# Kernel optimization log

Measured on AMD Instinct MI355X. Metric: run time of the kernel, lower is better.

The kernel has to match this reference:

```python
import jax, jax.numpy as jnp
import numpy as np


def setup_inputs() -> dict:
    key = jax.random.key(0)
    k1, k2 = jax.random.split(key)
    N, C, T, K = 8192, 3, 2048, 10
    Xt = jax.random.normal(k1, (N, C, T), dtype=jnp.float32)
    y_true = jax.random.randint(k2, (N,), 0, K, dtype=jnp.int64)
    return {"Xt": Xt, "y_true": y_true, "num_classes": K}


def reference(Xt, y_true, num_classes):
    # Within-Class Sum of Squares: for each class k,
    #   loss_k = mean((Xk - mean(Xk, axis=0))**2)  (mean over all elements)
    # total = mean over classes. Assumes all num_classes labels are present
    # (matches torch.unique iteration under this data distribution).
    N = Xt.shape[0]
    D = Xt.shape[1] * Xt.shape[2]  # elements per sample
    sums = jax.ops.segment_sum(Xt, y_true, num_segments=num_classes)        # [K, C, T]
    counts = jax.ops.segment_sum(jnp.ones((N,), Xt.dtype), y_true,
                                 num_segments=num_classes)                  # [K]
    means = sums / counts[:, None, None]                                    # [K, C, T]
    sq = jnp.square(Xt - means[y_true])                                     # [N, C, T]
    sq_per_sample = sq.reshape(N, -1).sum(axis=1)                           # [N]
    sq_sums = jax.ops.segment_sum(sq_per_sample, y_true,
                                  num_segments=num_classes)                 # [K]
    per_class_mse = sq_sums / (counts * D)                                  # [K]
    return per_class_mse.mean()
```

## Files before the change

### kernel.cpp

```cpp
#include <hip/hip_runtime.h>

#define N_SAMP 8192
#define D_DIM 6144
#define K_CLS 10
#define CHUNK 32
#define NWIN (N_SAMP / CHUNK)
#define COLS_PER_BLOCK 1024
#define NGROUPS (D_DIM / COLS_PER_BLOCK)
#define PIPE 8

__global__ __launch_bounds__(1024) void build_sort(const int* __restrict__ y,
                                                   int* __restrict__ counts,
                                                   int* __restrict__ sorted) {
    __shared__ int M[K_CLS * 1024];
    __shared__ int wsum[16];
    const int tid = threadIdx.x;
    const int lane = tid & 63;
    const int wid = tid >> 6;

    const int base = tid * 8;
    const int4 ya = ((const int4*)y)[tid * 2];
    const int4 yb = ((const int4*)y)[tid * 2 + 1];
    int yy[8] = {ya.x, ya.y, ya.z, ya.w, yb.x, yb.y, yb.z, yb.w};
    int h[K_CLS];
#pragma unroll
    for (int k = 0; k < K_CLS; ++k) h[k] = 0;
#pragma unroll
    for (int i = 0; i < 8; ++i)
#pragma unroll
        for (int k = 0; k < K_CLS; ++k) h[k] += (yy[i] == k) ? 1 : 0;
#pragma unroll
    for (int k = 0; k < K_CLS; ++k) M[k * 1024 + tid] = h[k];
    __syncthreads();

    int loc[K_CLS];
    int run = 0;
#pragma unroll
    for (int j = 0; j < K_CLS; ++j) { loc[j] = run; run += M[tid * K_CLS + j]; }
    int v = run;
#pragma unroll
    for (int d = 1; d < 64; d <<= 1) {
        int n = __shfl_up(v, d, 64);
        if (lane >= d) v += n;
    }
    if (lane == 63) wsum[wid] = v;
    __syncthreads();
    int wbase = 0;
#pragma unroll
    for (int w = 0; w < 16; ++w) wbase += (w < wid) ? wsum[w] : 0;
    const int tbase = wbase + (v - run);
    __syncthreads();
#pragma unroll
    for (int j = 0; j < K_CLS; ++j) M[tid * K_CLS + j] = tbase + loc[j];
    __syncthreads();

    if (tid < K_CLS) {
        const int s = M[tid * 1024];
        const int e = (tid == K_CLS - 1) ? N_SAMP : M[(tid + 1) * 1024];
        counts[tid] = e - s;
    }

    int off[K_CLS];
#pragma unroll
    for (int k = 0; k < K_CLS; ++k) off[k] = M[k * 1024 + tid];
#pragma unroll
    for (int i = 0; i < 8; ++i)
#pragma unroll
        for (int k = 0; k < K_CLS; ++k)
            if (yy[i] == k) sorted[off[k]++] = (k << 16) | (base + i);
}

__global__ __launch_bounds__(256) void wcss_accum(const float* __restrict__ X,
                                                  const int* __restrict__ sorted,
                                                  float* __restrict__ S1,
                                                  float* __restrict__ s2sum) {
    __shared__ int off_lds[CHUNK];
    __shared__ int cls_lds[CHUNK];
    __shared__ float wred[4];
    const int tid = threadIdx.x;
    const int lane = tid & 63;
    const int wid = tid >> 6;
    const int col0 = blockIdx.x * COLS_PER_BLOCK + tid * 4;

    if (tid < CHUNK) {
        const int p = sorted[blockIdx.y * CHUNK + tid];
        off_lds[tid] = (p & 0xffff) * (D_DIM * (int)sizeof(float));
        cls_lds[tid] = p >> 16;
    }
    __syncthreads();

    const char* basep = (const char*)(X + col0);
    float4 a1 = make_float4(0.f, 0.f, 0.f, 0.f);
    float s2c = 0.f;
    int kcur = __builtin_amdgcn_readfirstlane(cls_lds[0]);

    float4 buf[PIPE];
#pragma unroll
    for (int j = 0; j < PIPE; ++j)
        buf[j] = *(const float4*)(basep + (size_t)off_lds[j]);

#pragma unroll
    for (int s = 0; s < CHUNK; ++s) {
        const float4 v = buf[s & (PIPE - 1)];
        if (s + PIPE < CHUNK)
            buf[s & (PIPE - 1)] =
                *(const float4*)(basep + (size_t)off_lds[s + PIPE]);

        const int yk = __builtin_amdgcn_readfirstlane(cls_lds[s]);
        if (yk != kcur) {
            float* b1 = S1 + kcur * D_DIM + col0;
            atomicAdd(b1 + 0, a1.x); atomicAdd(b1 + 1, a1.y);
            atomicAdd(b1 + 2, a1.z); atomicAdd(b1 + 3, a1.w);
            float r = s2c;
#pragma unroll
            for (int o = 32; o > 0; o >>= 1) r += __shfl_down(r, o, 64);
            if (lane == 0) wred[wid] = r;
            __syncthreads();
            if (tid == 0)
                atomicAdd(&s2sum[kcur], wred[0] + wred[1] + wred[2] + wred[3]);
            __syncthreads();
            a1 = make_float4(0.f, 0.f, 0.f, 0.f);
            s2c = 0.f;
            kcur = yk;
        }
        a1.x += v.x; a1.y += v.y; a1.z += v.z; a1.w += v.w;
        s2c += v.x * v.x + v.y * v.y + v.z * v.z + v.w * v.w;
    }

    float* b1 = S1 + kcur * D_DIM + col0;
    atomicAdd(b1 + 0, a1.x); atomicAdd(b1 + 1, a1.y);
    atomicAdd(b1 + 2, a1.z); atomicAdd(b1 + 3, a1.w);
#pragma unroll
    for (int o = 32; o > 0; o >>= 1) s2c += __shfl_down(s2c, o, 64);
    if (lane == 0) wred[wid] = s2c;
    __syncthreads();
    if (tid == 0)
        atomicAdd(&s2sum[kcur], wred[0] + wred[1] + wred[2] + wred[3]);
}

__global__ __launch_bounds__(256) void wcss_finish(const float* __restrict__ S1,
                                                   const float* __restrict__ s2sum,
                                                   const int* __restrict__ counts,
                                                   float* __restrict__ out) {
    __shared__ float sbuf[256];
    const int tid = threadIdx.x;
    const int k = blockIdx.x / NGROUPS;
    const int g = blockIdx.x % NGROUPS;
    const float cnt = (float)counts[k];
    const float inv = 1.0f / (cnt * cnt * (float)D_DIM * (float)K_CLS);

    const float4 v = *(const float4*)(S1 + k * D_DIM + g * COLS_PER_BLOCK + tid * 4);
    float t = -(v.x * v.x + v.y * v.y + v.z * v.z + v.w * v.w) * inv;
    if (g == 0 && tid == 0)
        t += s2sum[k] / (cnt * (float)D_DIM * (float)K_CLS);

    sbuf[tid] = t;
    __syncthreads();
    for (int off = 128; off > 0; off >>= 1) {
        if (tid < off) sbuf[tid] += sbuf[tid + off];
        __syncthreads();
    }
    if (tid == 0) atomicAdd(out, sbuf[0]);
}

extern "C" void kernel_launch(void* const* d_in, const int* in_sizes, int n_in,
                              void* d_out, int out_size, void* d_ws, size_t ws_size,
                              hipStream_t stream) {
    const float* X = (const float*)d_in[0];
    const int* y = (const int*)d_in[1];

    float* S1 = (float*)d_ws;
    float* s2sum = S1 + K_CLS * D_DIM;
    int* counts = (int*)(s2sum + K_CLS);
    int* sorted = counts + K_CLS;
    float* out = (float*)d_out;

    hipMemsetAsync(S1, 0, (K_CLS * D_DIM + K_CLS) * sizeof(float), stream);
    hipMemsetAsync(out, 0, sizeof(float), stream);

    build_sort<<<dim3(1), dim3(1024), 0, stream>>>(y, counts, sorted);
    wcss_accum<<<dim3(NGROUPS, NWIN), dim3(256), 0, stream>>>(X, sorted, S1, s2sum);
    wcss_finish<<<dim3(K_CLS * NGROUPS), dim3(256), 0, stream>>>(S1, s2sum,
                                                                 counts, out);
}
```

Baseline: 298.3 us.

## Fold memsets into sort kernel and finish via last-block reduction

The two hipMemsetAsync calls are removed and the S1/s2sum zeroing moves into build_sort. The separate finish kernel is dropped in favour of a last-block-done pattern in wcss_accum: an atomic counter picks the final block, which reads S1 with atomic loads and writes the result directly. Loads of X become nontemporal. This cuts launch and memset overhead but serialises the final reduction onto one block of 256 threads reading 61K floats.

```diff
diff --git a/kernel.cpp b/kernel.cpp
--- a/kernel.cpp
+++ b/kernel.cpp
@@ -7,17 +7,33 @@
 #define NWIN (N_SAMP / CHUNK)
 #define COLS_PER_BLOCK 1024
 #define NGROUPS (D_DIM / COLS_PER_BLOCK)
+#define NBLK (NGROUPS * NWIN)
 #define PIPE 8
+
+typedef float f4 __attribute__((ext_vector_type(4)));
 
 __global__ __launch_bounds__(1024) void build_sort(const int* __restrict__ y,
                                                    int* __restrict__ counts,
-                                                   int* __restrict__ sorted) {
+                                                   int* __restrict__ sorted,
+                                                   float* __restrict__ S1,
+                                                   float* __restrict__ s2sum,
+                                                   unsigned* __restrict__ ctr) {
     __shared__ int M[K_CLS * 1024];
     __shared__ int wsum[16];
     const int tid = threadIdx.x;
     const int lane = tid & 63;
     const int wid = tid >> 6;
 
+    {
+        f4 z = {0.f, 0.f, 0.f, 0.f};
+        f4* p = (f4*)S1;
+#pragma unroll
+        for (int i = 0; i < (K_CLS * D_DIM) / (4 * 1024); ++i)
+            p[i * 1024 + tid] = z;
+        if (tid < K_CLS) s2sum[tid] = 0.f;
+        if (tid == K_CLS) *ctr = 0u;
+    }
+
     const int base = tid * 8;
     const int4 ya = ((const int4*)y)[tid * 2];
     const int4 yb = ((const int4*)y)[tid * 2 + 1];
@@ -72,11 +88,15 @@
 
 __global__ __launch_bounds__(256) void wcss_accum(const float* __restrict__ X,
                                                   const int* __restrict__ sorted,
+                                                  const int* __restrict__ counts,
                                                   float* __restrict__ S1,
-                                                  float* __restrict__ s2sum) {
+                                                  float* __restrict__ s2sum,
+                                                  unsigned* __restrict__ ctr,
+                                                  float* __restrict__ out) {
     __shared__ int off_lds[CHUNK];
     __shared__ int cls_lds[CHUNK];
     __shared__ float wred[4];
+    __shared__ int last_s;
     const int tid = threadIdx.x;
     const int lane = tid & 63;
     const int wid = tid >> 6;
@@ -90,21 +110,22 @@
     __syncthreads();
 
     const char* basep = (const char*)(X + col0);
-    float4 a1 = make_float4(0.f, 0.f, 0.f, 0.f);
+    f4 a1 = {0.f, 0.f, 0.f, 0.f};
     float s2c = 0.f;
     int kcur = __builtin_amdgcn_readfirstlane(cls_lds[0]);
 
-    float4 buf[PIPE];
+    f4 buf[PIPE];
 #pragma unroll
     for (int j = 0; j < PIPE; ++j)
-        buf[j] = *(const float4*)(basep + (size_t)off_lds[j]);
+        buf[j] = __builtin_nontemporal_load(
+            (const f4*)(basep + (size_t)off_lds[j]));
 
 #pragma unroll
     for (int s = 0; s < CHUNK; ++s) {
-        const float4 v = buf[s & (PIPE - 1)];
+        const f4 v = buf[s & (PIPE - 1)];
         if (s + PIPE < CHUNK)
-            buf[s & (PIPE - 1)] =
-                *(const float4*)(basep + (size_t)off_lds[s + PIPE]);
+            buf[s & (PIPE - 1)] = __builtin_nontemporal_load(
+                (const f4*)(basep + (size_t)off_lds[s + PIPE]));
 
         const int yk = __builtin_amdgcn_readfirstlane(cls_lds[s]);
         if (yk != kcur) {
@@ -119,11 +140,11 @@
             if (tid == 0)
                 atomicAdd(&s2sum[kcur], wred[0] + wred[1] + wred[2] + wred[3]);
             __syncthreads();
-            a1 = make_float4(0.f, 0.f, 0.f, 0.f);
+            a1 = (f4){0.f, 0.f, 0.f, 0.f};
             s2c = 0.f;
             kcur = yk;
         }
-        a1.x += v.x; a1.y += v.y; a1.z += v.z; a1.w += v.w;
+        a1 += v;
         s2c += v.x * v.x + v.y * v.y + v.z * v.z + v.w * v.w;
     }
 
@@ -136,31 +157,38 @@
     __syncthreads();
     if (tid == 0)
         atomicAdd(&s2sum[kcur], wred[0] + wred[1] + wred[2] + wred[3]);
-}
-
-__global__ __launch_bounds__(256) void wcss_finish(const float* __restrict__ S1,
-                                                   const float* __restrict__ s2sum,
-                                                   const int* __restrict__ counts,
-                                                   float* __restrict__ out) {
-    __shared__ float sbuf[256];
-    const int tid = threadIdx.x;
-    const int k = blockIdx.x / NGROUPS;
-    const int g = blockIdx.x % NGROUPS;
-    const float cnt = (float)counts[k];
-    const float inv = 1.0f / (cnt * cnt * (float)D_DIM * (float)K_CLS);
-
-    const float4 v = *(const float4*)(S1 + k * D_DIM + g * COLS_PER_BLOCK + tid * 4);
-    float t = -(v.x * v.x + v.y * v.y + v.z * v.z + v.w * v.w) * inv;
-    if (g == 0 && tid == 0)
-        t += s2sum[k] / (cnt * (float)D_DIM * (float)K_CLS);
-
-    sbuf[tid] = t;
-    __syncthreads();
-    for (int off = 128; off > 0; off >>= 1) {
-        if (tid < off) sbuf[tid] += sbuf[tid + off];
-        __syncthreads();
-    }
-    if (tid == 0) atomicAdd(out, sbuf[0]);
+
+    __threadfence();
+    if (tid == 0) {
+        unsigned t = atomicAdd(ctr, 1u);
+        last_s = (t == (unsigned)(NBLK - 1)) ? 1 : 0;
+    }
+    __syncthreads();
+    if (!last_s) return;
+    __threadfence();
+
+    float part = 0.f;
+#pragma unroll
+    for (int k = 0; k < K_CLS; ++k) {
+        const float c = (float)counts[k];
+        const float inv2 = 1.0f / (c * c * (float)D_DIM * (float)K_CLS);
+        const float* Sk = S1 + k * D_DIM;
+        for (int j = 0; j < D_DIM / 256; ++j) {
+            float vv = __hip_atomic_load(&Sk[j * 256 + tid], __ATOMIC_RELAXED,
+                                         __HIP_MEMORY_SCOPE_AGENT);
+            part -= vv * vv * inv2;
+        }
+        if (tid == 0)
+            part += __hip_atomic_load(&s2sum[k], __ATOMIC_RELAXED,
+                                      __HIP_MEMORY_SCOPE_AGENT) /
+                    (c * (float)D_DIM * (float)K_CLS);
+    }
+    float r = part;
+#pragma unroll
+    for (int o = 32; o > 0; o >>= 1) r += __shfl_down(r, o, 64);
+    if (lane == 0) wred[wid] = r;
+    __syncthreads();
+    if (tid == 0) *out = wred[0] + wred[1] + wred[2] + wred[3];
 }
 
 extern "C" void kernel_launch(void* const* d_in, const int* in_sizes, int n_in,
@@ -173,13 +201,11 @@
     float* s2sum = S1 + K_CLS * D_DIM;
     int* counts = (int*)(s2sum + K_CLS);
     int* sorted = counts + K_CLS;
+    unsigned* ctr = (unsigned*)(sorted + N_SAMP);
     float* out = (float*)d_out;
 
-    hipMemsetAsync(S1, 0, (K_CLS * D_DIM + K_CLS) * sizeof(float), stream);
-    hipMemsetAsync(out, 0, sizeof(float), stream);
-
-    build_sort<<<dim3(1), dim3(1024), 0, stream>>>(y, counts, sorted);
-    wcss_accum<<<dim3(NGROUPS, NWIN), dim3(256), 0, stream>>>(X, sorted, S1, s2sum);
-    wcss_finish<<<dim3(K_CLS * NGROUPS), dim3(256), 0, stream>>>(S1, s2sum,
-                                                                 counts, out);
+    build_sort<<<dim3(1), dim3(1024), 0, stream>>>(y, counts, sorted,
+                                                   S1, s2sum, ctr);
+    wcss_accum<<<dim3(NGROUPS, NWIN), dim3(256), 0, stream>>>(X, sorted, counts,
+                                                              S1, s2sum, ctr, out);
 }
```

Result: slower. 615.7 us (+106.4%).

## Replace sort-based gather with streaming masked per-class accumulation into partials

Applied to the files above, without the earlier changes.

Drops the counting sort and the gathered row reads. Rows are now streamed contiguously, and each thread keeps per-class accumulators selected by a 0/1 mask. Per-chunk partial sums are written to a workspace buffer and reduced in the finish kernel, which replaces the atomics on S1. The memsets are folded into the histogram kernel. The cost is ten accumulators per thread, which raises register pressure, plus about 31 MB of partial writes and reads.

```diff
diff --git a/kernel.cpp b/kernel.cpp
--- a/kernel.cpp
+++ b/kernel.cpp
@@ -3,25 +3,42 @@
 #define N_SAMP 8192
 #define D_DIM 6144
 #define K_CLS 10
-#define CHUNK 32
-#define NWIN (N_SAMP / CHUNK)
-#define COLS_PER_BLOCK 1024
-#define NGROUPS (D_DIM / COLS_PER_BLOCK)
-#define PIPE 8
+#define RCH 128
+#define ROWS_PER_CH (N_SAMP / RCH)
+#define CGS 2
+#define COLS_PER_CG (D_DIM / CGS)
+#define TPB_S (COLS_PER_CG / 4)
+#define FIN_CG 24
+#define FIN_COLS (D_DIM / FIN_CG)
 
-__global__ __launch_bounds__(1024) void build_sort(const int* __restrict__ y,
+typedef float f4 __attribute__((ext_vector_type(4)));
+
+__device__ __forceinline__ void atom_add_dev(float* p, float v) {
+    __hip_atomic_fetch_add(p, v, __ATOMIC_RELAXED, __HIP_MEMORY_SCOPE_AGENT);
+}
+__device__ __forceinline__ float wave_sum(float x) {
+#pragma unroll
+    for (int o = 32; o > 0; o >>= 1) x += __shfl_down(x, o, 64);
+    return x;
+}
+__device__ __forceinline__ int wave_sum_i(int x) {
+#pragma unroll
+    for (int o = 32; o > 0; o >>= 1) x += __shfl_down(x, o, 64);
+    return x;
+}
+
+__global__ __launch_bounds__(1024) void histo_init(const int* __restrict__ y,
                                                    int* __restrict__ counts,
-                                                   int* __restrict__ sorted) {
-    __shared__ int M[K_CLS * 1024];
-    __shared__ int wsum[16];
+                                                   float* __restrict__ s2sum,
+                                                   float* __restrict__ out) {
+    __shared__ int hred[16][K_CLS];
     const int tid = threadIdx.x;
     const int lane = tid & 63;
     const int wid = tid >> 6;
 
-    const int base = tid * 8;
     const int4 ya = ((const int4*)y)[tid * 2];
     const int4 yb = ((const int4*)y)[tid * 2 + 1];
-    int yy[8] = {ya.x, ya.y, ya.z, ya.w, yb.x, yb.y, yb.z, yb.w};
+    const int yy[8] = {ya.x, ya.y, ya.z, ya.w, yb.x, yb.y, yb.z, yb.w};
     int h[K_CLS];
 #pragma unroll
     for (int k = 0; k < K_CLS; ++k) h[k] = 0;
@@ -30,137 +47,85 @@
 #pragma unroll
         for (int k = 0; k < K_CLS; ++k) h[k] += (yy[i] == k) ? 1 : 0;
 #pragma unroll
-    for (int k = 0; k < K_CLS; ++k) M[k * 1024 + tid] = h[k];
+    for (int k = 0; k < K_CLS; ++k) {
+        const int s = wave_sum_i(h[k]);
+        if (lane == 0) hred[wid][k] = s;
+    }
     __syncthreads();
+    if (tid < K_CLS) {
+        int s = 0;
+#pragma unroll
+        for (int w = 0; w < 16; ++w) s += hred[w][tid];
+        counts[tid] = s;
+        s2sum[tid] = 0.f;
+    }
+    if (tid == K_CLS) *out = 0.f;
+}
 
-    int loc[K_CLS];
-    int run = 0;
+__global__ __launch_bounds__(TPB_S, 3) void wcss_stream(
+        const float* __restrict__ X, const int* __restrict__ y,
+        float* __restrict__ part, float* __restrict__ s2sum) {
+    const int tid = threadIdx.x;
+    const int lane = tid & 63;
+    const int cg = blockIdx.x;
+    const int rc = blockIdx.y;
+    const int col0 = cg * COLS_PER_CG + tid * 4;
+    const int rbase = rc * ROWS_PER_CH;
+
+    f4 acc[K_CLS];
+    float s2[K_CLS];
 #pragma unroll
-    for (int j = 0; j < K_CLS; ++j) { loc[j] = run; run += M[tid * K_CLS + j]; }
-    int v = run;
+    for (int k = 0; k < K_CLS; ++k) { acc[k] = (f4){0.f,0.f,0.f,0.f}; s2[k] = 0.f; }
+
+    const float* xp = X + (size_t)rbase * D_DIM + col0;
+    const int* yp = y + rbase;
+
+#pragma unroll 8
+    for (int r = 0; r < ROWS_PER_CH; ++r) {
+        const int yk = __builtin_amdgcn_readfirstlane(yp[r]);
+        const f4 v = *(const f4*)(xp + (size_t)r * D_DIM);
+        const float dot = v.x*v.x + v.y*v.y + v.z*v.z + v.w*v.w;
 #pragma unroll
-    for (int d = 1; d < 64; d <<= 1) {
-        int n = __shfl_up(v, d, 64);
-        if (lane >= d) v += n;
-    }
-    if (lane == 63) wsum[wid] = v;
-    __syncthreads();
-    int wbase = 0;
-#pragma unroll
-    for (int w = 0; w < 16; ++w) wbase += (w < wid) ? wsum[w] : 0;
-    const int tbase = wbase + (v - run);
-    __syncthreads();
-#pragma unroll
-    for (int j = 0; j < K_CLS; ++j) M[tid * K_CLS + j] = tbase + loc[j];
-    __syncthreads();
-
-    if (tid < K_CLS) {
-        const int s = M[tid * 1024];
-        const int e = (tid == K_CLS - 1) ? N_SAMP : M[(tid + 1) * 1024];
-        counts[tid] = e - s;
+        for (int k = 0; k < K_CLS; ++k) {
+            const float m = (yk == k) ? 1.0f : 0.0f;
+            acc[k] += v * m;
+            s2[k] = fmaf(m, dot, s2[k]);
+        }
     }
 
-    int off[K_CLS];
 #pragma unroll
-    for (int k = 0; k < K_CLS; ++k) off[k] = M[k * 1024 + tid];
+    for (int k = 0; k < K_CLS; ++k)
+        *(f4*)(part + ((size_t)(rc * K_CLS + k)) * D_DIM + col0) = acc[k];
+
 #pragma unroll
-    for (int i = 0; i < 8; ++i)
-#pragma unroll
-        for (int k = 0; k < K_CLS; ++k)
-            if (yy[i] == k) sorted[off[k]++] = (k << 16) | (base + i);
+    for (int k = 0; k < K_CLS; ++k) {
+        const float rs = wave_sum(s2[k]);
+        if (lane == 0) atom_add_dev(&s2sum[k], rs);
+    }
 }
 
-__global__ __launch_bounds__(256) void wcss_accum(const float* __restrict__ X,
-                                                  const int* __restrict__ sorted,
-                                                  float* __restrict__ S1,
-                                                  float* __restrict__ s2sum) {
-    __shared__ int off_lds[CHUNK];
-    __shared__ int cls_lds[CHUNK];
-    __shared__ float wred[4];
+__global__ __launch_bounds__(64) void wcss_finish(const float* __restrict__ part,
+                                                  const float* __restrict__ s2sum,
+                                                  const int* __restrict__ counts,
+                                                  float* __restrict__ out) {
     const int tid = threadIdx.x;
-    const int lane = tid & 63;
-    const int wid = tid >> 6;
-    const int col0 = blockIdx.x * COLS_PER_BLOCK + tid * 4;
+    const int k = blockIdx.x / FIN_CG;
+    const int g = blockIdx.x % FIN_CG;
+    const int col0 = g * FIN_COLS + tid * 4;
+    const float cnt = (float)counts[k];
+    const float invDK = 1.0f / ((float)D_DIM * (float)K_CLS);
 
-    if (tid < CHUNK) {
-        const int p = sorted[blockIdx.y * CHUNK + tid];
-        off_lds[tid] = (p & 0xffff) * (D_DIM * (int)sizeof(float));
-        cls_lds[tid] = p >> 16;
+    f4 S0 = {0.f,0.f,0.f,0.f}, S1v = {0.f,0.f,0.f,0.f};
+#pragma unroll 4
+    for (int rc = 0; rc < RCH; rc += 2) {
+        S0 += *(const f4*)(part + ((size_t)((rc    ) * K_CLS + k)) * D_DIM + col0);
+        S1v += *(const f4*)(part + ((size_t)((rc + 1) * K_CLS + k)) * D_DIM + col0);
     }
-    __syncthreads();
-
-    const char* basep = (const char*)(X + col0);
-    float4 a1 = make_float4(0.f, 0.f, 0.f, 0.f);
-    float s2c = 0.f;
-    int kcur = __builtin_amdgcn_readfirstlane(cls_lds[0]);
-
-    float4 buf[PIPE];
-#pragma unroll
-    for (int j = 0; j < PIPE; ++j)
-        buf[j] = *(const float4*)(basep + (size_t)off_lds[j]);
-
-#pragma unroll
-    for (int s = 0; s < CHUNK; ++s) {
-        const float4 v = buf[s & (PIPE - 1)];
-        if (s + PIPE < CHUNK)
-            buf[s & (PIPE - 1)] =
-                *(const float4*)(basep + (size_t)off_lds[s + PIPE]);
-
-        const int yk = __builtin_amdgcn_readfirstlane(cls_lds[s]);
-        if (yk != kcur) {
-            float* b1 = S1 + kcur * D_DIM + col0;
-            atomicAdd(b1 + 0, a1.x); atomicAdd(b1 + 1, a1.y);
-            atomicAdd(b1 + 2, a1.z); atomicAdd(b1 + 3, a1.w);
-            float r = s2c;
-#pragma unroll
-            for (int o = 32; o > 0; o >>= 1) r += __shfl_down(r, o, 64);
-            if (lane == 0) wred[wid] = r;
-            __syncthreads();
-            if (tid == 0)
-                atomicAdd(&s2sum[kcur], wred[0] + wred[1] + wred[2] + wred[3]);
-            __syncthreads();
-            a1 = make_float4(0.f, 0.f, 0.f, 0.f);
-            s2c = 0.f;
-            kcur = yk;
-        }
-        a1.x += v.x; a1.y += v.y; a1.z += v.z; a1.w += v.w;
-        s2c += v.x * v.x + v.y * v.y + v.z * v.z + v.w * v.w;
-    }
-
-    float* b1 = S1 + kcur * D_DIM + col0;
-    atomicAdd(b1 + 0, a1.x); atomicAdd(b1 + 1, a1.y);
-    atomicAdd(b1 + 2, a1.z); atomicAdd(b1 + 3, a1.w);
-#pragma unroll
-    for (int o = 32; o > 0; o >>= 1) s2c += __shfl_down(s2c, o, 64);
-    if (lane == 0) wred[wid] = s2c;
-    __syncthreads();
-    if (tid == 0)
-        atomicAdd(&s2sum[kcur], wred[0] + wred[1] + wred[2] + wred[3]);
-}
-
-__global__ __launch_bounds__(256) void wcss_finish(const float* __restrict__ S1,
-                                                   const float* __restrict__ s2sum,
-                                                   const int* __restrict__ counts,
-                                                   float* __restrict__ out) {
-    __shared__ float sbuf[256];
-    const int tid = threadIdx.x;
-    const int k = blockIdx.x / NGROUPS;
-    const int g = blockIdx.x % NGROUPS;
-    const float cnt = (float)counts[k];
-    const float inv = 1.0f / (cnt * cnt * (float)D_DIM * (float)K_CLS);
-
-    const float4 v = *(const float4*)(S1 + k * D_DIM + g * COLS_PER_BLOCK + tid * 4);
-    float t = -(v.x * v.x + v.y * v.y + v.z * v.z + v.w * v.w) * inv;
-    if (g == 0 && tid == 0)
-        t += s2sum[k] / (cnt * (float)D_DIM * (float)K_CLS);
-
-    sbuf[tid] = t;
-    __syncthreads();
-    for (int off = 128; off > 0; off >>= 1) {
-        if (tid < off) sbuf[tid] += sbuf[tid + off];
-        __syncthreads();
-    }
-    if (tid == 0) atomicAdd(out, sbuf[0]);
+    const f4 S = S0 + S1v;
+    float t = -(S.x*S.x + S.y*S.y + S.z*S.z + S.w*S.w) * invDK / (cnt * cnt);
+    if (g == 0 && tid == 0) t += s2sum[k] * invDK / cnt;
+    const float r = wave_sum(t);
+    if (tid == 0) atomicAdd(out, r);
 }
 
 extern "C" void kernel_launch(void* const* d_in, const int* in_sizes, int n_in,
@@ -169,17 +134,13 @@
     const float* X = (const float*)d_in[0];
     const int* y = (const int*)d_in[1];
 
-    float* S1 = (float*)d_ws;
-    float* s2sum = S1 + K_CLS * D_DIM;
+    float* part = (float*)d_ws;
+    float* s2sum = part + (size_t)RCH * K_CLS * D_DIM;
     int* counts = (int*)(s2sum + K_CLS);
-    int* sorted = counts + K_CLS;
     float* out = (float*)d_out;
 
-    hipMemsetAsync(S1, 0, (K_CLS * D_DIM + K_CLS) * sizeof(float), stream);
-    hipMemsetAsync(out, 0, sizeof(float), stream);
-
-    build_sort<<<dim3(1), dim3(1024), 0, stream>>>(y, counts, sorted);
-    wcss_accum<<<dim3(NGROUPS, NWIN), dim3(256), 0, stream>>>(X, sorted, S1, s2sum);
-    wcss_finish<<<dim3(K_CLS * NGROUPS), dim3(256), 0, stream>>>(S1, s2sum,
-                                                                 counts, out);
+    histo_init<<<dim3(1), dim3(1024), 0, stream>>>(y, counts, s2sum, out);
+    wcss_stream<<<dim3(CGS, RCH), dim3(TPB_S), 0, stream>>>(X, y, part, s2sum);
+    wcss_finish<<<dim3(K_CLS * FIN_CG), dim3(64), 0, stream>>>(part, s2sum,
+                                                               counts, out);
 }
```

Result: slower. 666.8 us (+123.5%).
